# Kernel optimization log

Hardware: AMD Instinct MI355X
Metric: run time of the kernel (lower is better)

The kernel has to match this reference:

```python
import jax, jax.numpy as jnp
import numpy as np

B, C, N, M, K = 1, 64, 65536, 65536, 16
H, O = 64, 128  # mlp hidden, out_channels


def setup_inputs() -> dict:
    key = jax.random.key(0)
    ks = jax.random.split(key, 8)
    return {
        "x": jax.random.normal(ks[0], (B, C, N), dtype=jnp.float32),
        "pos": jax.random.normal(ks[1], (B, 3, N), dtype=jnp.float32),
        "support_points": jax.random.normal(ks[2], (B, 3, M), dtype=jnp.float32),
        "W1": jax.random.normal(ks[3], (H, C + 3), dtype=jnp.float32) * 0.05,
        "b1": jax.random.normal(ks[4], (H,), dtype=jnp.float32) * 0.05,
        "W2": jax.random.normal(ks[5], (O, H), dtype=jnp.float32) * 0.05,
        "b2": jax.random.normal(ks[6], (O,), dtype=jnp.float32) * 0.05,
        "indices": jax.random.randint(ks[7], (B, M, K), 0, N, dtype=jnp.int64),
    }


def _gather_points(t, indices):
    # t: [B, C, N], indices: [B, M, K] -> [B, C, M, K]
    b, c, n = t.shape
    m, k = indices.shape[1], indices.shape[2]
    idx = indices.reshape(b, 1, m * k)  # broadcasts over channel dim
    return jnp.take_along_axis(t, idx, axis=2).reshape(b, c, m, k)


def reference(x, pos, support_points, W1, b1, W2, b2, indices):
    # gather neighbor features and positions: [B, C, M, K], [B, 3, M, K]
    feats = _gather_points(x, indices)
    pts = _gather_points(pos, indices) - support_points[:, :, :, None]
    h = jnp.concatenate([feats, pts], axis=1)  # [B, C+3, M, K]
    # shared per-point MLP (1x1 Conv2d == channel contraction)
    h = jnp.einsum("oc,bcmk->bomk", W1, h) + b1[None, :, None, None]
    h = jax.nn.relu(h)
    h = jnp.einsum("oc,bcmk->bomk", W2, h) + b2[None, :, None, None]
    # max-pool over neighborhood K -> [B, O, M]
    return jnp.max(h, axis=3)
```

## Files before the change

### kernel.cpp

```cpp
#include <hip/hip_runtime.h>

#define NPTS 65536
#define MPTS 65536

typedef __attribute__((ext_vector_type(8))) short bf16x8;
typedef __attribute__((ext_vector_type(4))) float f32x4;

__device__ __forceinline__ float bflo(unsigned int u){ union{unsigned int i; float f;} v; v.i = u<<16; return v.f; }
__device__ __forceinline__ float bfhi(unsigned int u){ union{unsigned int i; float f;} v; v.i = u & 0xffff0000u; return v.f; }
__device__ __forceinline__ unsigned short f2bf(float f){
  union{float f; unsigned int i;} v; v.f=f;
  unsigned int r = v.i + 0x7fffu + ((v.i>>16)&1u);
  return (unsigned short)(r>>16);
}
__device__ __forceinline__ unsigned int pk2(float a, float b){
  return (unsigned int)f2bf(a) | ((unsigned int)f2bf(b) << 16);
}

#define MFMA32(a,b,c) __builtin_amdgcn_mfma_f32_16x16x32_bf16((a),(b),(c),0,0,0)

__global__ __launch_bounds__(256) void pack_w(
    const float* __restrict__ W1, const float* __restrict__ W2,
    unsigned short* __restrict__ W1F, unsigned short* __restrict__ W2F) {
  const int wid = blockIdx.x * 256 + threadIdx.x;
  if (wid < 768) {
    const int f = wid >> 6, lane = wid & 63;
    const int q = lane >> 4, lr = lane & 15;
    if (f < 8) {
      const int kt = f >> 2, nt = f & 3;
      #pragma unroll
      for (int j = 0; j < 8; ++j)
        W1F[wid*8 + j] = f2bf(W1[(nt*16 + lr)*67 + kt*32 + q*8 + j]);
    } else {
      const int nt = f - 8;
      #pragma unroll
      for (int j = 0; j < 8; ++j) {
        const int c = 64 + q*4 + j;
        W1F[wid*8 + j] = (j < 4 && c < 67) ? f2bf(W1[(nt*16 + lr)*67 + c]) : (unsigned short)0;
      }
    }
  } else if (wid < 768 + 1024) {
    const int gg = wid - 768;
    const int g = gg >> 6, lane = gg & 63;
    const int q = lane >> 4, lr = lane & 15;
    const int kt = g >> 3, ot = g & 7;
    #pragma unroll
    for (int j = 0; j < 8; ++j)
      W2F[gg*8 + j] = f2bf(W2[(ot*16 + lr)*64 + kt*32 + q*8 + j]);
  }
}

__global__ __launch_bounds__(256) void pack_u(
    const float* __restrict__ x,
    const float* __restrict__ pos,
    const unsigned short* __restrict__ W1F,
    const float* __restrict__ b1,
    unsigned short* __restrict__ U) {
  const int t = threadIdx.x;
  const int lane = t & 63, w = t >> 6, quad = lane >> 4, lr = lane & 15;
  const int nb = blockIdx.x * 256 + w * 64;

  bf16x8 wa[2][4], wt[4];
  #pragma unroll
  for (int kt = 0; kt < 2; ++kt)
    #pragma unroll
    for (int nt = 0; nt < 4; ++nt)
      wa[kt][nt] = ((const bf16x8*)W1F)[(kt*4 + nt)*64 + lane];
  #pragma unroll
  for (int nt = 0; nt < 4; ++nt)
    wt[nt] = ((const bf16x8*)W1F)[(8 + nt)*64 + lane];

  const f32x4 fz = {0.f, 0.f, 0.f, 0.f};
  f32x4 acc[4][4];
  #pragma unroll
  for (int nt = 0; nt < 4; ++nt)
    #pragma unroll
    for (int pt = 0; pt < 4; ++pt) acc[nt][pt] = fz;

  #pragma unroll
  for (int kt = 0; kt < 2; ++kt) {
    bf16x8 bfr[4];
    #pragma unroll
    for (int pt = 0; pt < 4; ++pt) {
      const float* xc = x + (size_t)(kt*32 + quad*8) * NPTS + nb + pt*16 + lr;
      union { unsigned int d[4]; bf16x8 v; } mk;
      #pragma unroll
      for (int i = 0; i < 4; ++i)
        mk.d[i] = pk2(xc[(size_t)(2*i) * NPTS], xc[(size_t)(2*i + 1) * NPTS]);
      bfr[pt] = mk.v;
    }
    #pragma unroll
    for (int nt = 0; nt < 4; ++nt)
      #pragma unroll
      for (int pt = 0; pt < 4; ++pt)
        acc[nt][pt] = MFMA32(wa[kt][nt], bfr[pt], acc[nt][pt]);
  }
  {
    bf16x8 btr[4];
    #pragma unroll
    for (int pt = 0; pt < 4; ++pt) {
      const int n = nb + pt*16 + lr;
      union { unsigned int d[4]; bf16x8 v; } mk;
      mk.d[0] = pk2(pos[n], pos[NPTS + n]);
      mk.d[1] = (unsigned int)f2bf(pos[2*NPTS + n]);
      mk.d[2] = 0u; mk.d[3] = 0u;
      btr[pt] = mk.v;
    }
    #pragma unroll
    for (int nt = 0; nt < 4; ++nt)
      #pragma unroll
      for (int pt = 0; pt < 4; ++pt)
        acc[nt][pt] = MFMA32(wt[nt], btr[pt], acc[nt][pt]);
  }
  #pragma unroll
  for (int nt = 0; nt < 4; ++nt) {
    const float4 bb = *(const float4*)(b1 + nt*16 + quad*4);
    #pragma unroll
    for (int pt = 0; pt < 4; ++pt) {
      const int n = nb + pt*16 + lr;
      uint2 d;
      d.x = pk2(acc[nt][pt][0] + bb.x, acc[nt][pt][1] + bb.y);
      d.y = pk2(acc[nt][pt][2] + bb.z, acc[nt][pt][3] + bb.w);
      *(uint2*)(U + (size_t)n * 64 + nt*16 + quad*4) = d;
    }
  }
}

__global__ __launch_bounds__(256, 4) void pointnet_mfma2(
    const unsigned short* __restrict__ U,
    const float* __restrict__ sup,
    const float* __restrict__ W1,
    const unsigned short* __restrict__ W2F,
    const float* __restrict__ b2,
    const int* __restrict__ indices,
    float* __restrict__ out) {
  __shared__ __align__(16) unsigned short featB[256 * 72];

  const int t = threadIdx.x;
  const int m0 = blockIdx.x * 16;
  const int lane = t & 63, w = t >> 6, quad = lane >> 4, lr = lane & 15;

  {
    const int idx = indices[m0*16 + t];
    const uint4* src = (const uint4*)(U + (size_t)idx * 64);
    uint4 u[8];
    #pragma unroll
    for (int i = 0; i < 8; ++i) u[i] = src[i];
    uint4* dst = (uint4*)(featB + t * 72);
    #pragma unroll
    for (int i = 0; i < 8; ++i) dst[i] = u[i];
  }

  float w1p[16][3];
  #pragma unroll
  for (int kt = 0; kt < 2; ++kt)
    #pragma unroll
    for (int j = 0; j < 8; ++j) {
      const float* r = W1 + (size_t)(kt*32 + quad*8 + j) * 67 + 64;
      w1p[kt*8+j][0] = r[0]; w1p[kt*8+j][1] = r[1]; w1p[kt*8+j][2] = r[2];
    }

  bf16x8 ah[4][2];
  #pragma unroll
  for (int pt = 0; pt < 4; ++pt) {
    const int m = m0 + w*4 + pt;
    const float s0 = sup[m], s1 = sup[MPTS + m], s2 = sup[2*MPTS + m];
    #pragma unroll
    for (int kt = 0; kt < 2; ++kt) {
      const uint4 ur = *(const uint4*)&featB[(w*64 + pt*16 + lr)*72 + kt*32 + quad*8];
      const unsigned int uu[4] = {ur.x, ur.y, ur.z, ur.w};
      union { unsigned int d[4]; bf16x8 v; } mk;
      #pragma unroll
      for (int i = 0; i < 4; ++i) {
        const float* wl = w1p[kt*8 + 2*i];
        const float* wh = w1p[kt*8 + 2*i + 1];
        const float vl = wl[0]*s0 + wl[1]*s1 + wl[2]*s2;
        const float vh = wh[0]*s0 + wh[1]*s1 + wh[2]*s2;
        const float hl = fmaxf(bflo(uu[i]) - vl, 0.f);
        const float hh = fmaxf(bfhi(uu[i]) - vh, 0.f);
        mk.d[i] = pk2(hl, hh);
      }
      ah[pt][kt] = mk.v;
    }
  }

  const f32x4 fz = {0.f, 0.f, 0.f, 0.f};
  #pragma unroll
  for (int ot = 0; ot < 8; ++ot) {
    const bf16x8 wb0 = ((const bf16x8*)W2F)[(0*8 + ot)*64 + lane];
    const bf16x8 wb1 = ((const bf16x8*)W2F)[(1*8 + ot)*64 + lane];
    f32x4 a2[4];
    #pragma unroll
    for (int pt = 0; pt < 4; ++pt) {
      a2[pt] = MFMA32(ah[pt][0], wb0, fz);
      a2[pt] = MFMA32(ah[pt][1], wb1, a2[pt]);
    }
    float vm[4];
    #pragma unroll
    for (int pt = 0; pt < 4; ++pt) {
      float v = fmaxf(fmaxf(a2[pt][0], a2[pt][1]), fmaxf(a2[pt][2], a2[pt][3]));
      v = fmaxf(v, __shfl_xor(v, 16));
      v = fmaxf(v, __shfl_xor(v, 32));
      vm[pt] = v;
    }
    const float vq = (quad & 1) ? ((quad & 2) ? vm[3] : vm[1])
                                : ((quad & 2) ? vm[2] : vm[0]);
    const int o = ot*16 + lr;
    out[(size_t)o * MPTS + m0 + w*4 + quad] = vq + b2[o];
  }
}

__global__ __launch_bounds__(256) void pointnet_fallback(
    const float* __restrict__ x, const float* __restrict__ pos,
    const float* __restrict__ sup,
    const float* __restrict__ W1, const float* __restrict__ b1,
    const float* __restrict__ W2, const float* __restrict__ b2,
    const int* __restrict__ indices, float* __restrict__ out) {
  __shared__ float sfeat[16][68];
  __shared__ float shid[16][64];
  __shared__ float smax[4][128];
  __shared__ int sidx[16];
  const int t = threadIdx.x;
  const int m = blockIdx.x;
  if (t < 16) sidx[t] = indices[m*16 + t];
  const float sup0 = sup[m], sup1 = sup[MPTS + m], sup2 = sup[2*MPTS + m];
  __syncthreads();
  for (int u = t; u < 16*17; u += 256) {
    const int k = u / 17, c4 = (u - k*17) * 4;
    const int idx = sidx[k];
    float4 wv;
    if (c4 < 64) {
      wv.x = x[(size_t)(c4+0)*NPTS + idx]; wv.y = x[(size_t)(c4+1)*NPTS + idx];
      wv.z = x[(size_t)(c4+2)*NPTS + idx]; wv.w = x[(size_t)(c4+3)*NPTS + idx];
    } else {
      wv.x = pos[idx] - sup0; wv.y = pos[NPTS + idx] - sup1;
      wv.z = pos[2*NPTS + idx] - sup2; wv.w = 0.f;
    }
    *(float4*)&sfeat[k][c4] = wv;
  }
  const int h = t & 63, kg = t >> 6;
  float w1r[68];
  #pragma unroll
  for (int c = 0; c < 67; ++c) w1r[c] = W1[h*67 + c];
  w1r[67] = 0.f;
  const float bias1 = b1[h];
  __syncthreads();
  #pragma unroll
  for (int j = 0; j < 4; ++j) {
    const int k = kg*4 + j;
    float a = bias1;
    const float4* rr = (const float4*)sfeat[k];
    #pragma unroll
    for (int qq = 0; qq < 17; ++qq) {
      const float4 v = rr[qq];
      a += w1r[qq*4+0]*v.x + w1r[qq*4+1]*v.y + w1r[qq*4+2]*v.z + w1r[qq*4+3]*v.w;
    }
    shid[k][h] = fmaxf(a, 0.f);
  }
  const int ow = t & 63;
  float w2a[64], w2b[64];
  #pragma unroll
  for (int hh = 0; hh < 64; ++hh) { w2a[hh] = W2[ow*64 + hh]; w2b[hh] = W2[(ow+64)*64 + hh]; }
  __syncthreads();
  float mxa = -3.0e38f, mxb = -3.0e38f;
  #pragma unroll
  for (int j = 0; j < 4; ++j) {
    const int k = kg*4 + j;
    const float4* hr = (const float4*)shid[k];
    float pa = 0.f, pb = 0.f;
    #pragma unroll
    for (int qq = 0; qq < 16; ++qq) {
      const float4 v = hr[qq];
      pa += w2a[qq*4+0]*v.x + w2a[qq*4+1]*v.y + w2a[qq*4+2]*v.z + w2a[qq*4+3]*v.w;
      pb += w2b[qq*4+0]*v.x + w2b[qq*4+1]*v.y + w2b[qq*4+2]*v.z + w2b[qq*4+3]*v.w;
    }
    mxa = fmaxf(mxa, pa); mxb = fmaxf(mxb, pb);
  }
  smax[kg][ow] = mxa; smax[kg][64 + ow] = mxb;
  __syncthreads();
  if (t < 128) {
    out[(size_t)t * MPTS + m] =
        fmaxf(fmaxf(smax[0][t], smax[1][t]), fmaxf(smax[2][t], smax[3][t])) + b2[t];
  }
}

extern "C" void kernel_launch(void* const* d_in, const int* in_sizes, int n_in,
                              void* d_out, int out_size, void* d_ws, size_t ws_size,
                              hipStream_t stream) {
  const float* x   = (const float*)d_in[0];
  const float* pos = (const float*)d_in[1];
  const float* sup = (const float*)d_in[2];
  const float* W1  = (const float*)d_in[3];
  const float* b1  = (const float*)d_in[4];
  const float* W2  = (const float*)d_in[5];
  const float* b2  = (const float*)d_in[6];
  const int* indices = (const int*)d_in[7];
  float* out = (float*)d_out;

  const size_t U_BYTES   = (size_t)NPTS * 64 * 2;
  const size_t W1F_BYTES = 12 * 64 * 8 * 2;
  const size_t W2F_BYTES = 16 * 64 * 8 * 2;
  if (ws_size >= U_BYTES + W1F_BYTES + W2F_BYTES) {
    unsigned short* U   = (unsigned short*)d_ws;
    unsigned short* W1F = (unsigned short*)((char*)d_ws + U_BYTES);
    unsigned short* W2F = (unsigned short*)((char*)d_ws + U_BYTES + W1F_BYTES);
    pack_w<<<7, 256, 0, stream>>>(W1, W2, W1F, W2F);
    pack_u<<<NPTS/256, 256, 0, stream>>>(x, pos, W1F, b1, U);
    pointnet_mfma2<<<MPTS/16, 256, 0, stream>>>(U, sup, W1, W2F, b2, indices, out);
  } else {
    pointnet_fallback<<<MPTS, 256, 0, stream>>>(x, pos, sup, W1, b1, W2, b2, indices, out);
  }
}
```

Baseline: 142.9 us.

## Gather neighbor features into registers, pack W1 inline, shrink pack_u tiles

The main kernel now gathers each neighbor's precomputed first-layer row from global memory straight into the MFMA operand registers, dropping the shared-memory staging buffer. This removes LDS traffic and the LDS footprint, and the occupancy hint is raised from 4 to 5 blocks. The W1 packing kernel is removed, and pack_u converts W1 to bf16 itself while processing 16 points per wave instead of 64, which gives four times as many blocks. The costs are redundant per-block weight conversion in pack_u and possible register pressure from holding all gathered rows in registers.

```diff
diff --git a/kernel.cpp b/kernel.cpp
--- a/kernel.cpp
+++ b/kernel.cpp
@@ -19,30 +19,12 @@
 
 #define MFMA32(a,b,c) __builtin_amdgcn_mfma_f32_16x16x32_bf16((a),(b),(c),0,0,0)
 
-__global__ __launch_bounds__(256) void pack_w(
-    const float* __restrict__ W1, const float* __restrict__ W2,
-    unsigned short* __restrict__ W1F, unsigned short* __restrict__ W2F) {
-  const int wid = blockIdx.x * 256 + threadIdx.x;
-  if (wid < 768) {
-    const int f = wid >> 6, lane = wid & 63;
-    const int q = lane >> 4, lr = lane & 15;
-    if (f < 8) {
-      const int kt = f >> 2, nt = f & 3;
-      #pragma unroll
-      for (int j = 0; j < 8; ++j)
-        W1F[wid*8 + j] = f2bf(W1[(nt*16 + lr)*67 + kt*32 + q*8 + j]);
-    } else {
-      const int nt = f - 8;
-      #pragma unroll
-      for (int j = 0; j < 8; ++j) {
-        const int c = 64 + q*4 + j;
-        W1F[wid*8 + j] = (j < 4 && c < 67) ? f2bf(W1[(nt*16 + lr)*67 + c]) : (unsigned short)0;
-      }
-    }
-  } else if (wid < 768 + 1024) {
-    const int gg = wid - 768;
+__global__ __launch_bounds__(256) void pack_w2(
+    const float* __restrict__ W2, unsigned short* __restrict__ W2F) {
+  const int gg = blockIdx.x * 256 + threadIdx.x;
+  if (gg < 1024) {
     const int g = gg >> 6, lane = gg & 63;
-    const int q = lane >> 4, lr = lane & 15;
+    const int q = (lane & 63) >> 4, lr = lane & 15;
     const int kt = g >> 3, ot = g & 7;
     #pragma unroll
     for (int j = 0; j < 8; ++j)
@@ -53,80 +35,72 @@
 __global__ __launch_bounds__(256) void pack_u(
     const float* __restrict__ x,
     const float* __restrict__ pos,
-    const unsigned short* __restrict__ W1F,
+    const float* __restrict__ W1,
     const float* __restrict__ b1,
     unsigned short* __restrict__ U) {
   const int t = threadIdx.x;
   const int lane = t & 63, w = t >> 6, quad = lane >> 4, lr = lane & 15;
-  const int nb = blockIdx.x * 256 + w * 64;
+  const int nb = blockIdx.x * 64 + w * 16;
+  const int n = nb + lr;
 
   bf16x8 wa[2][4], wt[4];
   #pragma unroll
   for (int kt = 0; kt < 2; ++kt)
     #pragma unroll
+    for (int nt = 0; nt < 4; ++nt) {
+      const float* r = W1 + (size_t)(nt*16 + lr)*67 + kt*32 + quad*8;
+      const float4 a = *(const float4*)r;
+      const float4 b = *(const float4*)(r + 4);
+      union { unsigned int d[4]; bf16x8 v; } mk;
+      mk.d[0] = pk2(a.x, a.y); mk.d[1] = pk2(a.z, a.w);
+      mk.d[2] = pk2(b.x, b.y); mk.d[3] = pk2(b.z, b.w);
+      wa[kt][nt] = mk.v;
+    }
+  #pragma unroll
+  for (int nt = 0; nt < 4; ++nt) {
+    union { unsigned int d[4]; bf16x8 v; } mk;
+    mk.d[0] = 0u; mk.d[1] = 0u; mk.d[2] = 0u; mk.d[3] = 0u;
+    if (quad == 0) {
+      const float* r = W1 + (size_t)(nt*16 + lr)*67 + 64;
+      mk.d[0] = pk2(r[0], r[1]);
+      mk.d[1] = (unsigned int)f2bf(r[2]);
+    }
+    wt[nt] = mk.v;
+  }
+
+  const f32x4 fz = {0.f, 0.f, 0.f, 0.f};
+  f32x4 acc[4] = {fz, fz, fz, fz};
+  #pragma unroll
+  for (int kt = 0; kt < 2; ++kt) {
+    const float* xc = x + (size_t)(kt*32 + quad*8) * NPTS + n;
+    union { unsigned int d[4]; bf16x8 v; } mk;
+    #pragma unroll
+    for (int i = 0; i < 4; ++i)
+      mk.d[i] = pk2(xc[(size_t)(2*i) * NPTS], xc[(size_t)(2*i + 1) * NPTS]);
+    #pragma unroll
     for (int nt = 0; nt < 4; ++nt)
-      wa[kt][nt] = ((const bf16x8*)W1F)[(kt*4 + nt)*64 + lane];
-  #pragma unroll
-  for (int nt = 0; nt < 4; ++nt)
-    wt[nt] = ((const bf16x8*)W1F)[(8 + nt)*64 + lane];
-
-  const f32x4 fz = {0.f, 0.f, 0.f, 0.f};
-  f32x4 acc[4][4];
-  #pragma unroll
-  for (int nt = 0; nt < 4; ++nt)
-    #pragma unroll
-    for (int pt = 0; pt < 4; ++pt) acc[nt][pt] = fz;
-
-  #pragma unroll
-  for (int kt = 0; kt < 2; ++kt) {
-    bf16x8 bfr[4];
-    #pragma unroll
-    for (int pt = 0; pt < 4; ++pt) {
-      const float* xc = x + (size_t)(kt*32 + quad*8) * NPTS + nb + pt*16 + lr;
-      union { unsigned int d[4]; bf16x8 v; } mk;
-      #pragma unroll
-      for (int i = 0; i < 4; ++i)
-        mk.d[i] = pk2(xc[(size_t)(2*i) * NPTS], xc[(size_t)(2*i + 1) * NPTS]);
-      bfr[pt] = mk.v;
-    }
+      acc[nt] = MFMA32(wa[kt][nt], mk.v, acc[nt]);
+  }
+  {
+    union { unsigned int d[4]; bf16x8 v; } mk;
+    mk.d[0] = pk2(pos[n], pos[NPTS + n]);
+    mk.d[1] = (unsigned int)f2bf(pos[2*NPTS + n]);
+    mk.d[2] = 0u; mk.d[3] = 0u;
     #pragma unroll
     for (int nt = 0; nt < 4; ++nt)
-      #pragma unroll
-      for (int pt = 0; pt < 4; ++pt)
-        acc[nt][pt] = MFMA32(wa[kt][nt], bfr[pt], acc[nt][pt]);
-  }
-  {
-    bf16x8 btr[4];
-    #pragma unroll
-    for (int pt = 0; pt < 4; ++pt) {
-      const int n = nb + pt*16 + lr;
-      union { unsigned int d[4]; bf16x8 v; } mk;
-      mk.d[0] = pk2(pos[n], pos[NPTS + n]);
-      mk.d[1] = (unsigned int)f2bf(pos[2*NPTS + n]);
-      mk.d[2] = 0u; mk.d[3] = 0u;
-      btr[pt] = mk.v;
-    }
-    #pragma unroll
-    for (int nt = 0; nt < 4; ++nt)
-      #pragma unroll
-      for (int pt = 0; pt < 4; ++pt)
-        acc[nt][pt] = MFMA32(wt[nt], btr[pt], acc[nt][pt]);
+      acc[nt] = MFMA32(wt[nt], mk.v, acc[nt]);
   }
   #pragma unroll
   for (int nt = 0; nt < 4; ++nt) {
     const float4 bb = *(const float4*)(b1 + nt*16 + quad*4);
-    #pragma unroll
-    for (int pt = 0; pt < 4; ++pt) {
-      const int n = nb + pt*16 + lr;
-      uint2 d;
-      d.x = pk2(acc[nt][pt][0] + bb.x, acc[nt][pt][1] + bb.y);
-      d.y = pk2(acc[nt][pt][2] + bb.z, acc[nt][pt][3] + bb.w);
-      *(uint2*)(U + (size_t)n * 64 + nt*16 + quad*4) = d;
-    }
-  }
-}
-
-__global__ __launch_bounds__(256, 4) void pointnet_mfma2(
+    uint2 d;
+    d.x = pk2(acc[nt][0] + bb.x, acc[nt][1] + bb.y);
+    d.y = pk2(acc[nt][2] + bb.z, acc[nt][3] + bb.w);
+    *(uint2*)(U + (size_t)n * 64 + nt*16 + quad*4) = d;
+  }
+}
+
+__global__ __launch_bounds__(256, 5) void pointnet_reg(
     const unsigned short* __restrict__ U,
     const float* __restrict__ sup,
     const float* __restrict__ W1,
@@ -134,48 +108,47 @@
     const float* __restrict__ b2,
     const int* __restrict__ indices,
     float* __restrict__ out) {
-  __shared__ __align__(16) unsigned short featB[256 * 72];
-
   const int t = threadIdx.x;
   const int m0 = blockIdx.x * 16;
   const int lane = t & 63, w = t >> 6, quad = lane >> 4, lr = lane & 15;
-
-  {
-    const int idx = indices[m0*16 + t];
-    const uint4* src = (const uint4*)(U + (size_t)idx * 64);
-    uint4 u[8];
-    #pragma unroll
-    for (int i = 0; i < 8; ++i) u[i] = src[i];
-    uint4* dst = (uint4*)(featB + t * 72);
-    #pragma unroll
-    for (int i = 0; i < 8; ++i) dst[i] = u[i];
-  }
-
-  float w1p[16][3];
-  #pragma unroll
-  for (int kt = 0; kt < 2; ++kt)
+  const int wbase = m0 + w*4;
+
+  int idx[4];
+  #pragma unroll
+  for (int pt = 0; pt < 4; ++pt) idx[pt] = indices[(wbase + pt)*16 + lr];
+
+  uint4 ur[4][2];
+  #pragma unroll
+  for (int pt = 0; pt < 4; ++pt)
+    #pragma unroll
+    for (int kt = 0; kt < 2; ++kt)
+      ur[pt][kt] = *(const uint4*)(U + (size_t)idx[pt]*64 + kt*32 + quad*8);
+
+  float s0[4], s1[4], s2[4];
+  #pragma unroll
+  for (int pt = 0; pt < 4; ++pt) {
+    s0[pt] = sup[wbase + pt];
+    s1[pt] = sup[MPTS + wbase + pt];
+    s2[pt] = sup[2*MPTS + wbase + pt];
+  }
+
+  bf16x8 ah[4][2];
+  #pragma unroll
+  for (int kt = 0; kt < 2; ++kt) {
+    float w1p[8][3];
     #pragma unroll
     for (int j = 0; j < 8; ++j) {
-      const float* r = W1 + (size_t)(kt*32 + quad*8 + j) * 67 + 64;
-      w1p[kt*8+j][0] = r[0]; w1p[kt*8+j][1] = r[1]; w1p[kt*8+j][2] = r[2];
-    }
-
-  bf16x8 ah[4][2];
-  #pragma unroll
-  for (int pt = 0; pt < 4; ++pt) {
-    const int m = m0 + w*4 + pt;
-    const float s0 = sup[m], s1 = sup[MPTS + m], s2 = sup[2*MPTS + m];
-    #pragma unroll
-    for (int kt = 0; kt < 2; ++kt) {
-      const uint4 ur = *(const uint4*)&featB[(w*64 + pt*16 + lr)*72 + kt*32 + quad*8];
-      const unsigned int uu[4] = {ur.x, ur.y, ur.z, ur.w};
+      const float* r = W1 + (size_t)(kt*32 + quad*8 + j)*67 + 64;
+      w1p[j][0] = r[0]; w1p[j][1] = r[1]; w1p[j][2] = r[2];
+    }
+    #pragma unroll
+    for (int pt = 0; pt < 4; ++pt) {
+      const unsigned int uu[4] = {ur[pt][kt].x, ur[pt][kt].y, ur[pt][kt].z, ur[pt][kt].w};
       union { unsigned int d[4]; bf16x8 v; } mk;
       #pragma unroll
       for (int i = 0; i < 4; ++i) {
-        const float* wl = w1p[kt*8 + 2*i];
-        const float* wh = w1p[kt*8 + 2*i + 1];
-        const float vl = wl[0]*s0 + wl[1]*s1 + wl[2]*s2;
-        const float vh = wh[0]*s0 + wh[1]*s1 + wh[2]*s2;
+        const float vl = w1p[2*i][0]*s0[pt] + w1p[2*i][1]*s1[pt] + w1p[2*i][2]*s2[pt];
+        const float vh = w1p[2*i+1][0]*s0[pt] + w1p[2*i+1][1]*s1[pt] + w1p[2*i+1][2]*s2[pt];
         const float hl = fmaxf(bflo(uu[i]) - vl, 0.f);
         const float hh = fmaxf(bfhi(uu[i]) - vh, 0.f);
         mk.d[i] = pk2(hl, hh);
@@ -206,7 +179,7 @@
     const float vq = (quad & 1) ? ((quad & 2) ? vm[3] : vm[1])
                                 : ((quad & 2) ? vm[2] : vm[0]);
     const int o = ot*16 + lr;
-    out[(size_t)o * MPTS + m0 + w*4 + quad] = vq + b2[o];
+    out[(size_t)o * MPTS + wbase + quad] = vq + b2[o];
   }
 }
 
@@ -298,15 +271,13 @@
   float* out = (float*)d_out;
 
   const size_t U_BYTES   = (size_t)NPTS * 64 * 2;
-  const size_t W1F_BYTES = 12 * 64 * 8 * 2;
   const size_t W2F_BYTES = 16 * 64 * 8 * 2;
-  if (ws_size >= U_BYTES + W1F_BYTES + W2F_BYTES) {
+  if (ws_size >= U_BYTES + W2F_BYTES) {
     unsigned short* U   = (unsigned short*)d_ws;
-    unsigned short* W1F = (unsigned short*)((char*)d_ws + U_BYTES);
-    unsigned short* W2F = (unsigned short*)((char*)d_ws + U_BYTES + W1F_BYTES);
-    pack_w<<<7, 256, 0, stream>>>(W1, W2, W1F, W2F);
-    pack_u<<<NPTS/256, 256, 0, stream>>>(x, pos, W1F, b1, U);
-    pointnet_mfma2<<<MPTS/16, 256, 0, stream>>>(U, sup, W1, W2F, b2, indices, out);
+    unsigned short* W2F = (unsigned short*)((char*)d_ws + U_BYTES);
+    pack_w2<<<4, 256, 0, stream>>>(W2, W2F);
+    pack_u<<<NPTS/64, 256, 0, stream>>>(x, pos, W1, b1, U);
+    pointnet_reg<<<MPTS/16, 256, 0, stream>>>(U, sup, W1, W2F, b2, indices, out);
   } else {
     pointnet_fallback<<<MPTS, 256, 0, stream>>>(x, pos, sup, W1, b1, W2, b2, indices, out);
   }
```

Result: slower. 179.2 us (+25.4%).
